# Optimization experiments

Measured on AMD Instinct MI355X. Metric: run time of the kernel, lower is better.

## Reference

```python
import jax, jax.numpy as jnp
import numpy as np

B, L, V, D, C, R = 8, 2048, 32000, 512, 64, 64
NBLK = 2           # n_layers - 1
H = 2 * D          # stem hidden dim
STD = 0.02


def _ln(x, w, b):
    m = x.mean(-1, keepdims=True)
    v = ((x - m) ** 2).mean(-1, keepdims=True)
    return (x - m) / jnp.sqrt(v + 1e-5) * w + b


def setup_inputs() -> dict:
    key = jax.random.key(0)
    ks = jax.random.split(key, 16)
    n = lambda k, shp: jax.random.normal(k, shp, dtype=jnp.float32) * STD
    return {
        "token_ids": jax.random.randint(ks[0], (B, L), 0, V),
        "tok_emb": n(ks[1], (V, D)),
        "pos_emb": n(ks[2], (L, D)),
        "stem_ln_w": jnp.ones((NBLK, D), jnp.float32),
        "stem_ln_b": jnp.zeros((NBLK, D), jnp.float32),
        "stem_w1": n(ks[3], (NBLK, D, H)),
        "stem_b1": jnp.zeros((NBLK, H), jnp.float32),
        "stem_w2": n(ks[4], (NBLK, H, D)),
        "stem_b2": jnp.zeros((NBLK, D), jnp.float32),
        "role_ln_w": jnp.ones((D,), jnp.float32),
        "role_ln_b": jnp.zeros((D,), jnp.float32),
        "Wa": n(ks[5], (D, R)),
        "Wb": n(ks[6], (D, R)),
        "Wc": n(ks[7], (D, R)),
        "class_a": n(ks[8], (C, R)),
        "class_b": n(ks[9], (C, R)),
        "class_c": n(ks[10], (C, R)),
        "query_ln_w": jnp.ones((D,), jnp.float32),
        "query_ln_b": jnp.zeros((D,), jnp.float32),
        "Wq": n(ks[11], (D, C)),
        "bq": jnp.zeros((C,), jnp.float32),
    }


def reference(token_ids, tok_emb, pos_emb, stem_ln_w, stem_ln_b, stem_w1,
              stem_b1, stem_w2, stem_b2, role_ln_w, role_ln_b, Wa, Wb, Wc,
              class_a, class_b, class_c, query_ln_w, query_ln_b, Wq, bq):
    seq_len = token_ids.shape[1]
    x = tok_emb[token_ids] + pos_emb[:seq_len][None, :, :]  # [B,L,D]
    for i in range(NBLK):
        h = _ln(x, stem_ln_w[i], stem_ln_b[i])
        h = jax.nn.gelu(h @ stem_w1[i] + stem_b1[i], approximate=False)
        x = x + h @ stem_w2[i] + stem_b2[i]
    prefix = _ln(x[:, :-1], role_ln_w, role_ln_b)  # [B,L-1,D]
    a = jnp.tanh(prefix @ Wa)
    b = jnp.tanh(prefix @ Wb)
    c = jnp.tanh(prefix @ Wc)
    ua = jnp.einsum('blr,cr->blc', a, class_a)  # [B,L-1,C]
    ub = jnp.einsum('blr,cr->blc', b, class_b)
    uc = jnp.einsum('blr,cr->blc', c, class_c)
    # exact ordered-triplet sum  sum_{i<j<k} ua_i * ub_j * uc_k  via exclusive cumsums
    prefA = jnp.cumsum(ua, axis=1) - ua            # sum_{i<j} ua_i
    t = ub * prefA
    prefT = jnp.cumsum(t, axis=1) - t              # sum_{j<k} ub_j * prefA_j
    s = (uc * prefT).sum(axis=1)                   # [B,C]
    Lp = max(seq_len - 1, 1)
    denom = max(Lp * (Lp - 1) * (Lp - 2) / 6.0, 1.0)
    q = _ln(x[:, -1], query_ln_w, query_ln_b)
    return s / denom + q @ Wq + bq
```

## Files before the change

### kernel.cpp

```cpp
#include <hip/hip_runtime.h>

#define NROWS 16384
#define LSEQ  2048
#define NB    8

typedef short v8s __attribute__((ext_vector_type(8)));
typedef float v4f __attribute__((ext_vector_type(4)));

__device__ __forceinline__ unsigned short f2bf(float f) {
    unsigned int u = __float_as_uint(f);
    return (unsigned short)((u + 0x7fffu + ((u >> 16) & 1u)) >> 16);
}
__device__ __forceinline__ float bf2f(unsigned short u) {
    return __uint_as_float(((unsigned int)u) << 16);
}

__device__ __forceinline__ float fast_gelu(float v) {
    float z = fabsf(v) * 0.70710678118654752f;
    float t = __builtin_amdgcn_rcpf(1.0f + 0.3275911f * z);
    float poly = t * (0.254829592f + t * (-0.284496736f + t * (1.421413741f +
                 t * (-1.453152027f + t * 1.061405429f))));
    float erfz = 1.0f - poly * __expf(-z * z);
    float er = copysignf(erfz, v);
    return 0.5f * v * (1.0f + er);
}
__device__ __forceinline__ float fast_tanh(float y) {
    float e = __expf(2.0f * y);
    return (e - 1.0f) * __builtin_amdgcn_rcpf(e + 1.0f);
}

__global__ __launch_bounds__(256) void setup_kernel(
        const int* __restrict__ ids,
        const float* __restrict__ tok, const float* __restrict__ pos,
        const float* __restrict__ g0, const float* __restrict__ b0,
        unsigned short* __restrict__ x, unsigned short* __restrict__ hl,
        const float* __restrict__ w1, const float* __restrict__ w2,
        const float* __restrict__ wa, const float* __restrict__ wb, const float* __restrict__ wc,
        const float* __restrict__ ca, const float* __restrict__ cb, const float* __restrict__ cc,
        unsigned short* __restrict__ w1T, unsigned short* __restrict__ w2T,
        unsigned short* __restrict__ wabcT, unsigned short* __restrict__ clsb) {
    int blk = blockIdx.x;
    int t = threadIdx.x;
    if (blk < 4096) {
        int wave = t >> 6, lane = t & 63;
        long row = (long)blk * 4 + wave;
        int l = (int)(row & (LSEQ - 1));
        int id = ids[row];
        int d = lane * 8;
        float4 t0 = *(const float4*)(tok + (size_t)id * 512 + d);
        float4 t1 = *(const float4*)(tok + (size_t)id * 512 + d + 4);
        float4 p0 = *(const float4*)(pos + (size_t)l * 512 + d);
        float4 p1 = *(const float4*)(pos + (size_t)l * 512 + d + 4);
        float a[8] = {t0.x + p0.x, t0.y + p0.y, t0.z + p0.z, t0.w + p0.w,
                      t1.x + p1.x, t1.y + p1.y, t1.z + p1.z, t1.w + p1.w};
        unsigned int xp[4];
        #pragma unroll
        for (int i = 0; i < 4; ++i)
            xp[i] = (unsigned int)f2bf(a[2 * i]) | ((unsigned int)f2bf(a[2 * i + 1]) << 16);
        *(uint4*)(x + row * 512 + d) = *(uint4*)xp;
        float s = 0.f, s2 = 0.f;
        #pragma unroll
        for (int i = 0; i < 8; ++i) { s += a[i]; s2 += a[i] * a[i]; }
        #pragma unroll
        for (int o = 32; o > 0; o >>= 1) { s += __shfl_down(s, o); s2 += __shfl_down(s2, o); }
        s = __shfl(s, 0); s2 = __shfl(s2, 0);
        float m = s * (1.0f / 512.0f);
        float rinv = 1.0f / sqrtf(s2 * (1.0f / 512.0f) - m * m + 1e-5f);
        float4 ga = *(const float4*)(g0 + d), gb = *(const float4*)(g0 + d + 4);
        float4 ba = *(const float4*)(b0 + d), bb2 = *(const float4*)(b0 + d + 4);
        float gg[8] = {ga.x, ga.y, ga.z, ga.w, gb.x, gb.y, gb.z, gb.w};
        float bb[8] = {ba.x, ba.y, ba.z, ba.w, bb2.x, bb2.y, bb2.z, bb2.w};
        unsigned int hp[4];
        #pragma unroll
        for (int i = 0; i < 4; ++i) {
            unsigned short lo = f2bf((a[2 * i]     - m) * rinv * gg[2 * i]     + bb[2 * i]);
            unsigned short hi = f2bf((a[2 * i + 1] - m) * rinv * gg[2 * i + 1] + bb[2 * i + 1]);
            hp[i] = (unsigned int)lo | ((unsigned int)hi << 16);
        }
        *(uint4*)(hl + row * 512 + d) = *(uint4*)hp;
    } else if (blk < 6240) {
        int id = blk - 4096;
        int tx = t & 31, ty = t >> 5;
        const float* in; unsigned short* out; int R, C, bx, by, ldo;
        if (id < 1024) {
            int l = id >> 9, r = id & 511;
            in = w1 + l * 524288; out = w1T + l * 524288;
            R = 512; C = 1024; bx = r & 31; by = r >> 5; ldo = 512;
        } else if (id < 2048) {
            int l = (id - 1024) >> 9, r = (id - 1024) & 511;
            in = w2 + l * 524288; out = w2T + l * 524288;
            R = 1024; C = 512; bx = r & 15; by = r >> 4; ldo = 1024;
        } else {
            int g = (id - 2048) >> 5, r = (id - 2048) & 31;
            in = (g == 0) ? wa : (g == 1) ? wb : wc;
            out = wabcT + g * 32768;
            R = 512; C = 64; bx = r & 1; by = r >> 1; ldo = 512;
        }
        __shared__ unsigned short tile[32][33];
        int c0 = bx * 32, r0 = by * 32;
        for (int i = ty; i < 32; i += 8) {
            int r = r0 + i, c = c0 + tx;
            tile[i][tx] = (r < R && c < C) ? f2bf(in[(size_t)r * C + c]) : (unsigned short)0;
        }
        __syncthreads();
        for (int i = ty; i < 32; i += 8) {
            int c = c0 + i, r = r0 + tx;
            if (r < R && c < C) out[(size_t)c * ldo + r] = tile[tx][i];
        }
    } else {
        int g = blk - 6240;
        const float* src = (g == 0) ? ca : (g == 1) ? cb : cc;
        unsigned short* dst = clsb + g * 4096;
        for (int i = t; i < 4096; i += 256) dst[i] = f2bf(src[i]);
    }
}

__global__ __launch_bounds__(256) void ln_kernel(const unsigned short* __restrict__ x,
        const float* __restrict__ g, const float* __restrict__ b,
        unsigned short* __restrict__ out) {
    int wave = threadIdx.x >> 6, lane = threadIdx.x & 63;
    long row = (long)blockIdx.x * 4 + wave;
    int d = lane * 8;
    uint4 xp = *(const uint4*)(x + row * 512 + d);
    const unsigned int* xw = (const unsigned int*)&xp;
    float a[8];
    #pragma unroll
    for (int i = 0; i < 4; ++i) {
        a[2 * i]     = bf2f((unsigned short)(xw[i] & 0xffff));
        a[2 * i + 1] = bf2f((unsigned short)(xw[i] >> 16));
    }
    float s = 0.f, s2 = 0.f;
    #pragma unroll
    for (int i = 0; i < 8; ++i) { s += a[i]; s2 += a[i] * a[i]; }
    #pragma unroll
    for (int o = 32; o > 0; o >>= 1) { s += __shfl_down(s, o); s2 += __shfl_down(s2, o); }
    s = __shfl(s, 0); s2 = __shfl(s2, 0);
    float m = s * (1.0f / 512.0f);
    float rinv = 1.0f / sqrtf(s2 * (1.0f / 512.0f) - m * m + 1e-5f);
    float4 g0 = *(const float4*)(g + d), g1 = *(const float4*)(g + d + 4);
    float4 b0 = *(const float4*)(b + d), b1 = *(const float4*)(b + d + 4);
    float gg[8] = {g0.x, g0.y, g0.z, g0.w, g1.x, g1.y, g1.z, g1.w};
    float bb[8] = {b0.x, b0.y, b0.z, b0.w, b1.x, b1.y, b1.z, b1.w};
    unsigned int hp[4];
    #pragma unroll
    for (int i = 0; i < 4; ++i) {
        unsigned short lo = f2bf((a[2 * i]     - m) * rinv * gg[2 * i]     + bb[2 * i]);
        unsigned short hi = f2bf((a[2 * i + 1] - m) * rinv * gg[2 * i + 1] + bb[2 * i + 1]);
        hp[i] = (unsigned int)lo | ((unsigned int)hi << 16);
    }
    *(uint4*)(out + row * 512 + d) = *(uint4*)hp;
}

#define EPI_GELU_BF16  0
#define EPI_RES_BF16   1

template <int EPI, int TN>
__global__ __launch_bounds__(256) void gemm_r2(
        const unsigned short* __restrict__ A, int lda,
        const unsigned short* __restrict__ BT, int ldb,
        const float* __restrict__ bias,
        const unsigned short* __restrict__ xres,
        unsigned short* __restrict__ Cout, int ldc, int K) {
    constexpr int NJ = TN / 32;
    __shared__ unsigned short As[128][40] __attribute__((aligned(16)));
    __shared__ unsigned short Bs[TN][40] __attribute__((aligned(16)));
    const int t = threadIdx.x;
    const int lane = t & 63, wave = t >> 6;
    const int quad = lane >> 4, l16 = lane & 15;
    const int wm = (wave >> 1) * 64, wn = (wave & 1) * (TN / 2);
    const long tileM = (long)blockIdx.x * 128, tileN = (long)blockIdx.y * TN;
    const int arow = t >> 2, acol = (t & 3) * 8;

    const unsigned short* gA0 = A + (tileM + arow) * lda + acol;
    const unsigned short* gA1 = gA0 + 64 * (long)lda;
    const unsigned short* gB0 = BT + (tileN + arow) * ldb + acol;
    const unsigned short* gB1 = gB0 + 64 * (long)ldb;

    v4f acc[4][NJ] = {};
    uint4 a0, a1, b0, b1;

    a0 = *(const uint4*)gA0; a1 = *(const uint4*)gA1; gA0 += 32; gA1 += 32;
    b0 = *(const uint4*)gB0; gB0 += 32;
    if (TN == 128) { b1 = *(const uint4*)gB1; gB1 += 32; }
    *(uint4*)&As[arow][acol] = a0;
    *(uint4*)&As[arow + 64][acol] = a1;
    *(uint4*)&Bs[arow][acol] = b0;
    if (TN == 128) *(uint4*)&Bs[arow + 64][acol] = b1;

    const int nk = K >> 5;
    for (int kk = 0; kk < nk; ++kk) {
        __syncthreads();
        const bool more = kk + 1 < nk;
        if (more) {
            a0 = *(const uint4*)gA0; a1 = *(const uint4*)gA1; gA0 += 32; gA1 += 32;
            b0 = *(const uint4*)gB0; gB0 += 32;
            if (TN == 128) { b1 = *(const uint4*)gB1; gB1 += 32; }
        }
        v8s af[4], bfr[NJ];
        #pragma unroll
        for (int i = 0; i < 4; ++i) af[i] = *(const v8s*)&As[wm + i * 16 + l16][quad * 8];
        #pragma unroll
        for (int j = 0; j < NJ; ++j) bfr[j] = *(const v8s*)&Bs[wn + j * 16 + l16][quad * 8];
        #pragma unroll
        for (int i = 0; i < 4; ++i)
            #pragma unroll
            for (int j = 0; j < NJ; ++j)
                acc[i][j] = __builtin_amdgcn_mfma_f32_16x16x32_bf16(bfr[j], af[i], acc[i][j], 0, 0, 0);
        __syncthreads();
        if (more) {
            *(uint4*)&As[arow][acol] = a0;
            *(uint4*)&As[arow + 64][acol] = a1;
            *(uint4*)&Bs[arow][acol] = b0;
            if (TN == 128) *(uint4*)&Bs[arow + 64][acol] = b1;
        }
    }

    #pragma unroll
    for (int i = 0; i < 4; ++i) {
        long m = tileM + wm + i * 16 + l16;
        #pragma unroll
        for (int j = 0; j < NJ; ++j) {
            long n0 = tileN + wn + j * 16 + quad * 4;
            float4 bi = *(const float4*)&bias[n0];
            const float* bip = (const float*)&bi;
            unsigned short pk[4];
            if (EPI == EPI_GELU_BF16) {
                #pragma unroll
                for (int r = 0; r < 4; ++r)
                    pk[r] = f2bf(fast_gelu(acc[i][j][r] + bip[r]));
            } else {
                ushort4 xr4 = *(const ushort4*)&xres[m * ldc + n0];
                const unsigned short* xp = (const unsigned short*)&xr4;
                #pragma unroll
                for (int r = 0; r < 4; ++r)
                    pk[r] = f2bf(acc[i][j][r] + bip[r] + bf2f(xp[r]));
            }
            *(ushort4*)&Cout[m * ldc + n0] = *(ushort4*)pk;
        }
    }
}

__global__ __launch_bounds__(256) void tanh_class_kernel(
        const unsigned short* __restrict__ A,
        const unsigned short* __restrict__ WT,
        const unsigned short* __restrict__ cls,
        unsigned short* __restrict__ uu) {
    __shared__ unsigned short As[128][40] __attribute__((aligned(16)));
    __shared__ unsigned short Bs[64][40] __attribute__((aligned(16)));
    __shared__ unsigned short P[128 * 72] __attribute__((aligned(16)));
    const int t = threadIdx.x;
    const int lane = t & 63, wave = t >> 6;
    const int quad = lane >> 4, l16 = lane & 15;
    const int wm = (wave >> 1) * 64, wn = (wave & 1) * 32;
    const long tileM = (long)blockIdx.x * 128;
    const int g = blockIdx.y;
    const int arow = t >> 2, acol = (t & 3) * 8;

    const unsigned short* BT = WT + g * 32768;
    v8s cf[2][2];
    #pragma unroll
    for (int ks = 0; ks < 2; ++ks)
        #pragma unroll
        for (int j = 0; j < 2; ++j)
            cf[ks][j] = *(const v8s*)&cls[g * 4096 + (wn + j * 16 + l16) * 64 + ks * 32 + quad * 8];

    const unsigned short* gA0 = A + (tileM + arow) * 512 + acol;
    const unsigned short* gA1 = gA0 + 64 * 512;
    const unsigned short* gB0 = BT + arow * 512 + acol;

    v4f acc[4][2] = {};
    uint4 a0, a1, b0;
    a0 = *(const uint4*)gA0; a1 = *(const uint4*)gA1; gA0 += 32; gA1 += 32;
    b0 = *(const uint4*)gB0; gB0 += 32;
    *(uint4*)&As[arow][acol] = a0;
    *(uint4*)&As[arow + 64][acol] = a1;
    *(uint4*)&Bs[arow][acol] = b0;

    for (int kk = 0; kk < 16; ++kk) {
        __syncthreads();
        const bool more = kk < 15;
        if (more) {
            a0 = *(const uint4*)gA0; a1 = *(const uint4*)gA1; gA0 += 32; gA1 += 32;
            b0 = *(const uint4*)gB0; gB0 += 32;
        }
        v8s af[4], bfr[2];
        #pragma unroll
        for (int i = 0; i < 4; ++i) af[i] = *(const v8s*)&As[wm + i * 16 + l16][quad * 8];
        #pragma unroll
        for (int j = 0; j < 2; ++j) bfr[j] = *(const v8s*)&Bs[wn + j * 16 + l16][quad * 8];
        #pragma unroll
        for (int i = 0; i < 4; ++i)
            #pragma unroll
            for (int j = 0; j < 2; ++j)
                acc[i][j] = __builtin_amdgcn_mfma_f32_16x16x32_bf16(bfr[j], af[i], acc[i][j], 0, 0, 0);
        __syncthreads();
        if (more) {
            *(uint4*)&As[arow][acol] = a0;
            *(uint4*)&As[arow + 64][acol] = a1;
            *(uint4*)&Bs[arow][acol] = b0;
        }
    }

    #pragma unroll
    for (int i = 0; i < 4; ++i) {
        int m = wm + i * 16 + l16;
        #pragma unroll
        for (int j = 0; j < 2; ++j) {
            int n0 = wn + j * 16 + quad * 4;
            unsigned short pk[4];
            #pragma unroll
            for (int r = 0; r < 4; ++r) pk[r] = f2bf(fast_tanh(acc[i][j][r]));
            *(ushort4*)&P[m * 72 + n0] = *(ushort4*)pk;
        }
    }
    __syncthreads();

    v4f acc2[4][2] = {};
    #pragma unroll
    for (int ks = 0; ks < 2; ++ks) {
        v8s paf[4];
        #pragma unroll
        for (int i = 0; i < 4; ++i)
            paf[i] = *(const v8s*)&P[(wm + i * 16 + l16) * 72 + ks * 32 + quad * 8];
        #pragma unroll
        for (int i = 0; i < 4; ++i)
            #pragma unroll
            for (int j = 0; j < 2; ++j)
                acc2[i][j] = __builtin_amdgcn_mfma_f32_16x16x32_bf16(cf[ks][j], paf[i], acc2[i][j], 0, 0, 0);
    }

    #pragma unroll
    for (int i = 0; i < 4; ++i) {
        long m = tileM + wm + i * 16 + l16;
        #pragma unroll
        for (int j = 0; j < 2; ++j) {
            int c0 = wn + j * 16 + quad * 4;
            unsigned short pk[4];
            #pragma unroll
            for (int r = 0; r < 4; ++r) pk[r] = f2bf(acc2[i][j][r]);
            *(ushort4*)&uu[m * 192 + g * 64 + c0] = *(ushort4*)pk;
        }
    }
}

__global__ __launch_bounds__(64) void scan_part_kernel(const unsigned short* __restrict__ u,
                                                       float* __restrict__ part) {
    int b = blockIdx.x, seg = blockIdx.y;
    int c = threadIdx.x;
    int l0 = seg * 32;
    int l1 = l0 + 32; if (l1 > 2047) l1 = 2047;
    float sA = 0.f, sB = 0.f, sC = 0.f, T = 0.f, M = 0.f, U = 0.f;
    const unsigned short* base = u + ((size_t)b * LSEQ + l0) * 192 + c;
    for (int l = l0; l < l1; ++l) {
        float ua = bf2f(base[0]), ub = bf2f(base[64]), uc = bf2f(base[128]);
        base += 192;
        U += uc * T;
        M += uc * sB;
        T += ub * sA;
        sA += ua; sB += ub; sC += uc;
    }
    float* p = part + ((size_t)(b * 64 + seg)) * 384 + c;
    p[0] = sA; p[64] = sB; p[128] = sC; p[192] = T; p[256] = M; p[320] = U;
}

__global__ __launch_bounds__(64) void combine_final_kernel(const float* __restrict__ part,
        const unsigned short* __restrict__ x,
        const float* __restrict__ qw, const float* __restrict__ qb,
        const float* __restrict__ Wq, const float* __restrict__ bq,
        float* __restrict__ out, float inv_denom) {
    int b = blockIdx.x;
    int c = threadIdx.x;
    const float* p = part + (size_t)b * 64 * 384 + c;
    float A = p[0], B = p[64], Tt = p[192], Mt = p[256], Ut = p[320];
    for (int seg = 1; seg < 64; ++seg) {
        const float* q2 = p + seg * 384;
        float a2 = q2[0], b2 = q2[64], c2 = q2[128], t2 = q2[192], m2 = q2[256], u2 = q2[320];
        float Un = Ut + u2 + c2 * Tt + A * m2;
        float Tn = Tt + t2 + A * b2;
        float Mn = Mt + m2 + B * c2;
        A += a2; B += b2;
        Ut = Un; Tt = Tn; Mt = Mn;
    }
    __shared__ float q[512];
    __shared__ float mv[2];
    const unsigned short* xr = x + ((size_t)b * LSEQ + (LSEQ - 1)) * 512;
    float s1 = 0.f, s2 = 0.f;
    for (int i = c; i < 512; i += 64) { float v = bf2f(xr[i]); q[i] = v; s1 += v; s2 += v * v; }
    #pragma unroll
    for (int o = 32; o > 0; o >>= 1) { s1 += __shfl_down(s1, o); s2 += __shfl_down(s2, o); }
    if (c == 0) {
        float m = s1 * (1.0f / 512.0f);
        float var = s2 * (1.0f / 512.0f) - m * m;
        mv[0] = m; mv[1] = 1.0f / sqrtf(var + 1e-5f);
    }
    __syncthreads();
    float m = mv[0], r = mv[1];
    for (int i = c; i < 512; i += 64) q[i] = (q[i] - m) * r * qw[i] + qb[i];
    __syncthreads();
    float acc = 0.f;
    for (int d = 0; d < 512; ++d) acc += q[d] * Wq[d * 64 + c];
    out[b * 64 + c] = Ut * inv_denom + acc + bq[c];
}

extern "C" void kernel_launch(void* const* d_in, const int* in_sizes, int n_in,
                              void* d_out, int out_size, void* d_ws, size_t ws_size,
                              hipStream_t stream) {
    const int*   token_ids   = (const int*)d_in[0];
    const float* tok_emb     = (const float*)d_in[1];
    const float* pos_emb     = (const float*)d_in[2];
    const float* stem_ln_w   = (const float*)d_in[3];
    const float* stem_ln_b   = (const float*)d_in[4];
    const float* stem_w1     = (const float*)d_in[5];
    const float* stem_b1     = (const float*)d_in[6];
    const float* stem_w2     = (const float*)d_in[7];
    const float* stem_b2     = (const float*)d_in[8];
    const float* role_ln_w   = (const float*)d_in[9];
    const float* role_ln_b   = (const float*)d_in[10];
    const float* Wa          = (const float*)d_in[11];
    const float* Wb          = (const float*)d_in[12];
    const float* Wc          = (const float*)d_in[13];
    const float* class_a     = (const float*)d_in[14];
    const float* class_b     = (const float*)d_in[15];
    const float* class_c     = (const float*)d_in[16];
    const float* query_ln_w  = (const float*)d_in[17];
    const float* query_ln_b  = (const float*)d_in[18];
    const float* Wq          = (const float*)d_in[19];
    const float* bq          = (const float*)d_in[20];
    float* out = (float*)d_out;

    char* wsb = (char*)d_ws;
    unsigned short* x    = (unsigned short*)(wsb);
    unsigned short* hl   = (unsigned short*)(wsb + 16777216);
    unsigned short* Hb   = (unsigned short*)(wsb + 33554432);
    unsigned short* uu   = (unsigned short*)(wsb + 67108864);
    float* part          = (float*)(wsb + 73400320);
    unsigned short* w1T  = (unsigned short*)(wsb + 74188800);
    unsigned short* w2T  = (unsigned short*)(wsb + 76285952);
    unsigned short* wabcT= (unsigned short*)(wsb + 78383104);
    unsigned short* clsb = (unsigned short*)(wsb + 78579712);

    setup_kernel<<<6243, 256, 0, stream>>>(token_ids, tok_emb, pos_emb,
        stem_ln_w, stem_ln_b, x, hl,
        stem_w1, stem_w2, Wa, Wb, Wc, class_a, class_b, class_c,
        w1T, w2T, wabcT, clsb);

    for (int i = 0; i < 2; ++i) {
        if (i > 0)
            ln_kernel<<<NROWS / 4, 256, 0, stream>>>(x, stem_ln_w + 512, stem_ln_b + 512, hl);
        gemm_r2<EPI_GELU_BF16, 128><<<dim3(128, 8), 256, 0, stream>>>(
            hl, 512, w1T + i * 524288, 512, stem_b1 + i * 1024, nullptr, Hb, 1024, 512);
        gemm_r2<EPI_RES_BF16, 64><<<dim3(128, 8), 256, 0, stream>>>(
            Hb, 1024, w2T + i * 524288, 1024, stem_b2 + i * 512, x, x, 512, 1024);
    }

    ln_kernel<<<NROWS / 4, 256, 0, stream>>>(x, role_ln_w, role_ln_b, hl);

    tanh_class_kernel<<<dim3(128, 3), 256, 0, stream>>>(hl, wabcT, clsb, uu);

    scan_part_kernel<<<dim3(NB, 64), 64, 0, stream>>>(uu, part);

    float inv_denom = (float)(6.0 / (2047.0 * 2046.0 * 2045.0));
    combine_final_kernel<<<NB, 64, 0, stream>>>(part, x, query_ln_w, query_ln_b,
                                                Wq, bq, out, inv_denom);
}
```

Before: 343.4 us.

## Fuse LayerNorm into GEMM prologues by folding gamma/beta into weights

Removes the standalone LayerNorm kernels and the hl intermediate buffer. LayerNorm gamma is folded into the transposed weights and beta is precomputed into the biases during setup, so the GEMMs only need the per-row mean and rstd. Each GEMM block computes these statistics from x in a prologue and normalizes A tiles as it loads them. The cost is that every N-tile block recomputes the row statistics (8x redundant reads of x for W1, 3x for the tanh/class kernel), and the bias precompute loops run serially in setup.

```diff
diff --git a/kernel.cpp b/kernel.cpp
--- a/kernel.cpp
+++ b/kernel.cpp
@@ -29,16 +29,31 @@
     return (e - 1.0f) * __builtin_amdgcn_rcpf(e + 1.0f);
 }
 
+__device__ __forceinline__ uint4 ln8(uint4 v, float m, float r) {
+    const unsigned int* vw = (const unsigned int*)&v;
+    unsigned int o[4];
+    #pragma unroll
+    for (int k = 0; k < 4; ++k) {
+        float f0 = (bf2f((unsigned short)(vw[k] & 0xffff)) - m) * r;
+        float f1 = (bf2f((unsigned short)(vw[k] >> 16)) - m) * r;
+        o[k] = (unsigned int)f2bf(f0) | ((unsigned int)f2bf(f1) << 16);
+    }
+    return *(uint4*)o;
+}
+
 __global__ __launch_bounds__(256) void setup_kernel(
         const int* __restrict__ ids,
         const float* __restrict__ tok, const float* __restrict__ pos,
-        const float* __restrict__ g0, const float* __restrict__ b0,
-        unsigned short* __restrict__ x, unsigned short* __restrict__ hl,
+        unsigned short* __restrict__ x,
         const float* __restrict__ w1, const float* __restrict__ w2,
         const float* __restrict__ wa, const float* __restrict__ wb, const float* __restrict__ wc,
         const float* __restrict__ ca, const float* __restrict__ cb, const float* __restrict__ cc,
+        const float* __restrict__ lnw, const float* __restrict__ lnb,
+        const float* __restrict__ sb1,
+        const float* __restrict__ rlw, const float* __restrict__ rlb,
         unsigned short* __restrict__ w1T, unsigned short* __restrict__ w2T,
-        unsigned short* __restrict__ wabcT, unsigned short* __restrict__ clsb) {
+        unsigned short* __restrict__ wabcT, unsigned short* __restrict__ clsb,
+        float* __restrict__ b1p, float* __restrict__ babc) {
     int blk = blockIdx.x;
     int t = threadIdx.x;
     if (blk < 4096) {
@@ -58,33 +73,14 @@
         for (int i = 0; i < 4; ++i)
             xp[i] = (unsigned int)f2bf(a[2 * i]) | ((unsigned int)f2bf(a[2 * i + 1]) << 16);
         *(uint4*)(x + row * 512 + d) = *(uint4*)xp;
-        float s = 0.f, s2 = 0.f;
-        #pragma unroll
-        for (int i = 0; i < 8; ++i) { s += a[i]; s2 += a[i] * a[i]; }
-        #pragma unroll
-        for (int o = 32; o > 0; o >>= 1) { s += __shfl_down(s, o); s2 += __shfl_down(s2, o); }
-        s = __shfl(s, 0); s2 = __shfl(s2, 0);
-        float m = s * (1.0f / 512.0f);
-        float rinv = 1.0f / sqrtf(s2 * (1.0f / 512.0f) - m * m + 1e-5f);
-        float4 ga = *(const float4*)(g0 + d), gb = *(const float4*)(g0 + d + 4);
-        float4 ba = *(const float4*)(b0 + d), bb2 = *(const float4*)(b0 + d + 4);
-        float gg[8] = {ga.x, ga.y, ga.z, ga.w, gb.x, gb.y, gb.z, gb.w};
-        float bb[8] = {ba.x, ba.y, ba.z, ba.w, bb2.x, bb2.y, bb2.z, bb2.w};
-        unsigned int hp[4];
-        #pragma unroll
-        for (int i = 0; i < 4; ++i) {
-            unsigned short lo = f2bf((a[2 * i]     - m) * rinv * gg[2 * i]     + bb[2 * i]);
-            unsigned short hi = f2bf((a[2 * i + 1] - m) * rinv * gg[2 * i + 1] + bb[2 * i + 1]);
-            hp[i] = (unsigned int)lo | ((unsigned int)hi << 16);
-        }
-        *(uint4*)(hl + row * 512 + d) = *(uint4*)hp;
     } else if (blk < 6240) {
         int id = blk - 4096;
         int tx = t & 31, ty = t >> 5;
         const float* in; unsigned short* out; int R, C, bx, by, ldo;
+        const float* sc = nullptr;
         if (id < 1024) {
             int l = id >> 9, r = id & 511;
-            in = w1 + l * 524288; out = w1T + l * 524288;
+            in = w1 + l * 524288; out = w1T + l * 524288; sc = lnw + l * 512;
             R = 512; C = 1024; bx = r & 31; by = r >> 5; ldo = 512;
         } else if (id < 2048) {
             int l = (id - 1024) >> 9, r = (id - 1024) & 511;
@@ -93,125 +89,127 @@
         } else {
             int g = (id - 2048) >> 5, r = (id - 2048) & 31;
             in = (g == 0) ? wa : (g == 1) ? wb : wc;
-            out = wabcT + g * 32768;
+            out = wabcT + g * 32768; sc = rlw;
             R = 512; C = 64; bx = r & 1; by = r >> 1; ldo = 512;
         }
         __shared__ unsigned short tile[32][33];
         int c0 = bx * 32, r0 = by * 32;
         for (int i = ty; i < 32; i += 8) {
             int r = r0 + i, c = c0 + tx;
-            tile[i][tx] = (r < R && c < C) ? f2bf(in[(size_t)r * C + c]) : (unsigned short)0;
+            if (r < R && c < C) {
+                float f = in[(size_t)r * C + c];
+                if (sc) f *= sc[r];
+                tile[i][tx] = f2bf(f);
+            } else tile[i][tx] = 0;
         }
         __syncthreads();
         for (int i = ty; i < 32; i += 8) {
             int c = c0 + i, r = r0 + tx;
             if (r < R && c < C) out[(size_t)c * ldo + r] = tile[tx][i];
         }
-    } else {
+    } else if (blk < 6243) {
         int g = blk - 6240;
         const float* src = (g == 0) ? ca : (g == 1) ? cb : cc;
         unsigned short* dst = clsb + g * 4096;
         for (int i = t; i < 4096; i += 256) dst[i] = f2bf(src[i]);
-    }
-}
-
-__global__ __launch_bounds__(256) void ln_kernel(const unsigned short* __restrict__ x,
-        const float* __restrict__ g, const float* __restrict__ b,
-        unsigned short* __restrict__ out) {
-    int wave = threadIdx.x >> 6, lane = threadIdx.x & 63;
-    long row = (long)blockIdx.x * 4 + wave;
-    int d = lane * 8;
-    uint4 xp = *(const uint4*)(x + row * 512 + d);
-    const unsigned int* xw = (const unsigned int*)&xp;
-    float a[8];
-    #pragma unroll
-    for (int i = 0; i < 4; ++i) {
-        a[2 * i]     = bf2f((unsigned short)(xw[i] & 0xffff));
-        a[2 * i + 1] = bf2f((unsigned short)(xw[i] >> 16));
-    }
-    float s = 0.f, s2 = 0.f;
-    #pragma unroll
-    for (int i = 0; i < 8; ++i) { s += a[i]; s2 += a[i] * a[i]; }
-    #pragma unroll
-    for (int o = 32; o > 0; o >>= 1) { s += __shfl_down(s, o); s2 += __shfl_down(s2, o); }
-    s = __shfl(s, 0); s2 = __shfl(s2, 0);
-    float m = s * (1.0f / 512.0f);
-    float rinv = 1.0f / sqrtf(s2 * (1.0f / 512.0f) - m * m + 1e-5f);
-    float4 g0 = *(const float4*)(g + d), g1 = *(const float4*)(g + d + 4);
-    float4 b0 = *(const float4*)(b + d), b1 = *(const float4*)(b + d + 4);
-    float gg[8] = {g0.x, g0.y, g0.z, g0.w, g1.x, g1.y, g1.z, g1.w};
-    float bb[8] = {b0.x, b0.y, b0.z, b0.w, b1.x, b1.y, b1.z, b1.w};
-    unsigned int hp[4];
-    #pragma unroll
-    for (int i = 0; i < 4; ++i) {
-        unsigned short lo = f2bf((a[2 * i]     - m) * rinv * gg[2 * i]     + bb[2 * i]);
-        unsigned short hi = f2bf((a[2 * i + 1] - m) * rinv * gg[2 * i + 1] + bb[2 * i + 1]);
-        hp[i] = (unsigned int)lo | ((unsigned int)hi << 16);
-    }
-    *(uint4*)(out + row * 512 + d) = *(uint4*)hp;
-}
-
-#define EPI_GELU_BF16  0
-#define EPI_RES_BF16   1
-
-template <int EPI, int TN>
-__global__ __launch_bounds__(256) void gemm_r2(
-        const unsigned short* __restrict__ A, int lda,
-        const unsigned short* __restrict__ BT, int ldb,
+    } else if (blk < 6251) {
+        int gidx = (blk - 6243) * 256 + t;
+        int i = gidx >> 10, n = gidx & 1023;
+        float sum = sb1[i * 1024 + n];
+        const float* lb = lnb + i * 512;
+        const float* wp = w1 + i * 524288 + n;
+        for (int c = 0; c < 512; ++c) sum += lb[c] * wp[(size_t)c * 1024];
+        b1p[gidx] = sum;
+    } else {
+        if (t < 192) {
+            int g = t >> 6, r = t & 63;
+            const float* wp = ((g == 0) ? wa : (g == 1) ? wb : wc) + r;
+            float sum = 0.f;
+            for (int c = 0; c < 512; ++c) sum += rlb[c] * wp[(size_t)c * 64];
+            babc[t] = sum;
+        }
+    }
+}
+
+__global__ __launch_bounds__(256) void gemm_w1ln(
+        const unsigned short* __restrict__ X,
+        const unsigned short* __restrict__ BT,
         const float* __restrict__ bias,
-        const unsigned short* __restrict__ xres,
-        unsigned short* __restrict__ Cout, int ldc, int K) {
-    constexpr int NJ = TN / 32;
+        unsigned short* __restrict__ Cout) {
     __shared__ unsigned short As[128][40] __attribute__((aligned(16)));
-    __shared__ unsigned short Bs[TN][40] __attribute__((aligned(16)));
+    __shared__ unsigned short Bs[128][40] __attribute__((aligned(16)));
+    __shared__ float mS[128], rSS[128];
     const int t = threadIdx.x;
     const int lane = t & 63, wave = t >> 6;
     const int quad = lane >> 4, l16 = lane & 15;
-    const int wm = (wave >> 1) * 64, wn = (wave & 1) * (TN / 2);
-    const long tileM = (long)blockIdx.x * 128, tileN = (long)blockIdx.y * TN;
+    const int wm = (wave >> 1) * 64, wn = (wave & 1) * 64;
+    const long tileM = (long)blockIdx.x * 128, tileN = (long)blockIdx.y * 128;
     const int arow = t >> 2, acol = (t & 3) * 8;
 
-    const unsigned short* gA0 = A + (tileM + arow) * lda + acol;
-    const unsigned short* gA1 = gA0 + 64 * (long)lda;
-    const unsigned short* gB0 = BT + (tileN + arow) * ldb + acol;
-    const unsigned short* gB1 = gB0 + 64 * (long)ldb;
-
-    v4f acc[4][NJ] = {};
+    {
+        int sr = t >> 1, sh = t & 1;
+        const unsigned short* xr = X + (tileM + sr) * 512 + sh * 256;
+        float s = 0.f, s2 = 0.f;
+        #pragma unroll 8
+        for (int q = 0; q < 32; ++q) {
+            uint4 v = *(const uint4*)(xr + q * 8);
+            const unsigned int* vw = (const unsigned int*)&v;
+            #pragma unroll
+            for (int k = 0; k < 4; ++k) {
+                float f0 = bf2f((unsigned short)(vw[k] & 0xffff));
+                float f1 = bf2f((unsigned short)(vw[k] >> 16));
+                s += f0 + f1; s2 += f0 * f0 + f1 * f1;
+            }
+        }
+        s += __shfl_xor(s, 1); s2 += __shfl_xor(s2, 1);
+        if (sh == 0) {
+            float m = s * (1.0f / 512.0f);
+            mS[sr] = m;
+            rSS[sr] = 1.0f / sqrtf(s2 * (1.0f / 512.0f) - m * m + 1e-5f);
+        }
+    }
+    __syncthreads();
+    const float m0 = mS[arow],      r0 = rSS[arow];
+    const float m1 = mS[arow + 64], r1 = rSS[arow + 64];
+
+    const unsigned short* gA0 = X + (tileM + arow) * 512 + acol;
+    const unsigned short* gA1 = gA0 + 64 * 512;
+    const unsigned short* gB0 = BT + (tileN + arow) * 512 + acol;
+    const unsigned short* gB1 = gB0 + 64 * 512;
+
+    v4f acc[4][4] = {};
     uint4 a0, a1, b0, b1;
 
     a0 = *(const uint4*)gA0; a1 = *(const uint4*)gA1; gA0 += 32; gA1 += 32;
-    b0 = *(const uint4*)gB0; gB0 += 32;
-    if (TN == 128) { b1 = *(const uint4*)gB1; gB1 += 32; }
-    *(uint4*)&As[arow][acol] = a0;
-    *(uint4*)&As[arow + 64][acol] = a1;
-    *(uint4*)&Bs[arow][acol] = b0;
-    if (TN == 128) *(uint4*)&Bs[arow + 64][acol] = b1;
-
-    const int nk = K >> 5;
-    for (int kk = 0; kk < nk; ++kk) {
-        __syncthreads();
-        const bool more = kk + 1 < nk;
+    b0 = *(const uint4*)gB0; b1 = *(const uint4*)gB1; gB0 += 32; gB1 += 32;
+    *(uint4*)&As[arow][acol]      = ln8(a0, m0, r0);
+    *(uint4*)&As[arow + 64][acol] = ln8(a1, m1, r1);
+    *(uint4*)&Bs[arow][acol]      = b0;
+    *(uint4*)&Bs[arow + 64][acol] = b1;
+
+    for (int kk = 0; kk < 16; ++kk) {
+        __syncthreads();
+        const bool more = kk < 15;
         if (more) {
             a0 = *(const uint4*)gA0; a1 = *(const uint4*)gA1; gA0 += 32; gA1 += 32;
-            b0 = *(const uint4*)gB0; gB0 += 32;
-            if (TN == 128) { b1 = *(const uint4*)gB1; gB1 += 32; }
-        }
-        v8s af[4], bfr[NJ];
+            b0 = *(const uint4*)gB0; b1 = *(const uint4*)gB1; gB0 += 32; gB1 += 32;
+        }
+        v8s af[4], bfr[4];
         #pragma unroll
         for (int i = 0; i < 4; ++i) af[i] = *(const v8s*)&As[wm + i * 16 + l16][quad * 8];
         #pragma unroll
-        for (int j = 0; j < NJ; ++j) bfr[j] = *(const v8s*)&Bs[wn + j * 16 + l16][quad * 8];
+        for (int j = 0; j < 4; ++j) bfr[j] = *(const v8s*)&Bs[wn + j * 16 + l16][quad * 8];
         #pragma unroll
         for (int i = 0; i < 4; ++i)
             #pragma unroll
-            for (int j = 0; j < NJ; ++j)
+            for (int j = 0; j < 4; ++j)
                 acc[i][j] = __builtin_amdgcn_mfma_f32_16x16x32_bf16(bfr[j], af[i], acc[i][j], 0, 0, 0);
         __syncthreads();
         if (more) {
-            *(uint4*)&As[arow][acol] = a0;
-            *(uint4*)&As[arow + 64][acol] = a1;
-            *(uint4*)&Bs[arow][acol] = b0;
-            if (TN == 128) *(uint4*)&Bs[arow + 64][acol] = b1;
+            *(uint4*)&As[arow][acol]      = ln8(a0, m0, r0);
+            *(uint4*)&As[arow + 64][acol] = ln8(a1, m1, r1);
+            *(uint4*)&Bs[arow][acol]      = b0;
+            *(uint4*)&Bs[arow + 64][acol] = b1;
         }
     }
 
@@ -219,35 +217,99 @@
     for (int i = 0; i < 4; ++i) {
         long m = tileM + wm + i * 16 + l16;
         #pragma unroll
-        for (int j = 0; j < NJ; ++j) {
+        for (int j = 0; j < 4; ++j) {
             long n0 = tileN + wn + j * 16 + quad * 4;
             float4 bi = *(const float4*)&bias[n0];
             const float* bip = (const float*)&bi;
             unsigned short pk[4];
-            if (EPI == EPI_GELU_BF16) {
-                #pragma unroll
-                for (int r = 0; r < 4; ++r)
-                    pk[r] = f2bf(fast_gelu(acc[i][j][r] + bip[r]));
-            } else {
-                ushort4 xr4 = *(const ushort4*)&xres[m * ldc + n0];
-                const unsigned short* xp = (const unsigned short*)&xr4;
-                #pragma unroll
-                for (int r = 0; r < 4; ++r)
-                    pk[r] = f2bf(acc[i][j][r] + bip[r] + bf2f(xp[r]));
-            }
-            *(ushort4*)&Cout[m * ldc + n0] = *(ushort4*)pk;
+            #pragma unroll
+            for (int r = 0; r < 4; ++r)
+                pk[r] = f2bf(fast_gelu(acc[i][j][r] + bip[r]));
+            *(ushort4*)&Cout[m * 1024 + n0] = *(ushort4*)pk;
+        }
+    }
+}
+
+__global__ __launch_bounds__(256) void gemm_w2(
+        const unsigned short* __restrict__ A,
+        const unsigned short* __restrict__ BT,
+        const float* __restrict__ bias,
+        unsigned short* __restrict__ Xio) {
+    __shared__ unsigned short As[128][40] __attribute__((aligned(16)));
+    __shared__ unsigned short Bs[64][40] __attribute__((aligned(16)));
+    const int t = threadIdx.x;
+    const int lane = t & 63, wave = t >> 6;
+    const int quad = lane >> 4, l16 = lane & 15;
+    const int wm = (wave >> 1) * 64, wn = (wave & 1) * 32;
+    const long tileM = (long)blockIdx.x * 128, tileN = (long)blockIdx.y * 64;
+    const int arow = t >> 2, acol = (t & 3) * 8;
+
+    const unsigned short* gA0 = A + (tileM + arow) * 1024 + acol;
+    const unsigned short* gA1 = gA0 + 64 * 1024;
+    const unsigned short* gB0 = BT + (tileN + arow) * 1024 + acol;
+    v4f acc[4][2] = {};
+    uint4 a0, a1, b0;
+
+    a0 = *(const uint4*)gA0; a1 = *(const uint4*)gA1; gA0 += 32; gA1 += 32;
+    b0 = *(const uint4*)gB0; gB0 += 32;
+    *(uint4*)&As[arow][acol] = a0;
+    *(uint4*)&As[arow + 64][acol] = a1;
+    if (arow < 64) *(uint4*)&Bs[arow][acol] = b0;
+
+    for (int kk = 0; kk < 32; ++kk) {
+        __syncthreads();
+        const bool more = kk < 31;
+        if (more) {
+            a0 = *(const uint4*)gA0; a1 = *(const uint4*)gA1; gA0 += 32; gA1 += 32;
+            b0 = *(const uint4*)gB0; gB0 += 32;
+        }
+        v8s af[4], bfr[2];
+        #pragma unroll
+        for (int i = 0; i < 4; ++i) af[i] = *(const v8s*)&As[wm + i * 16 + l16][quad * 8];
+        #pragma unroll
+        for (int j = 0; j < 2; ++j) bfr[j] = *(const v8s*)&Bs[wn + j * 16 + l16][quad * 8];
+        #pragma unroll
+        for (int i = 0; i < 4; ++i)
+            #pragma unroll
+            for (int j = 0; j < 2; ++j)
+                acc[i][j] = __builtin_amdgcn_mfma_f32_16x16x32_bf16(bfr[j], af[i], acc[i][j], 0, 0, 0);
+        __syncthreads();
+        if (more) {
+            *(uint4*)&As[arow][acol] = a0;
+            *(uint4*)&As[arow + 64][acol] = a1;
+            if (arow < 64) *(uint4*)&Bs[arow][acol] = b0;
+        }
+    }
+
+    #pragma unroll
+    for (int i = 0; i < 4; ++i) {
+        long m = tileM + wm + i * 16 + l16;
+        #pragma unroll
+        for (int j = 0; j < 2; ++j) {
+            long n0 = tileN + wn + j * 16 + quad * 4;
+            float4 bi = *(const float4*)&bias[n0];
+            const float* bip = (const float*)&bi;
+            ushort4 xr4 = *(const ushort4*)&Xio[m * 512 + n0];
+            const unsigned short* xp = (const unsigned short*)&xr4;
+            unsigned short pk[4];
+            #pragma unroll
+            for (int r = 0; r < 4; ++r)
+                pk[r] = f2bf(acc[i][j][r] + bip[r] + bf2f(xp[r]));
+            *(ushort4*)&Xio[m * 512 + n0] = *(ushort4*)pk;
         }
     }
 }
 
 __global__ __launch_bounds__(256) void tanh_class_kernel(
-        const unsigned short* __restrict__ A,
+        const unsigned short* __restrict__ X,
         const unsigned short* __restrict__ WT,
         const unsigned short* __restrict__ cls,
+        const float* __restrict__ babc,
         unsigned short* __restrict__ uu) {
     __shared__ unsigned short As[128][40] __attribute__((aligned(16)));
     __shared__ unsigned short Bs[64][40] __attribute__((aligned(16)));
     __shared__ unsigned short P[128 * 72] __attribute__((aligned(16)));
+    __shared__ float mS[128], rSS[128];
     const int t = threadIdx.x;
     const int lane = t & 63, wave = t >> 6;
     const int quad = lane >> 4, l16 = lane & 15;
@@ -256,6 +318,32 @@
     const int g = blockIdx.y;
     const int arow = t >> 2, acol = (t & 3) * 8;
 
+    {
+        int sr = t >> 1, sh = t & 1;
+        const unsigned short* xr = X + (tileM + sr) * 512 + sh * 256;
+        float s = 0.f, s2 = 0.f;
+        #pragma unroll 8
+        for (int q = 0; q < 32; ++q) {
+            uint4 v = *(const uint4*)(xr + q * 8);
+            const unsigned int* vw = (const unsigned int*)&v;
+            #pragma unroll
+            for (int k = 0; k < 4; ++k) {
+                float f0 = bf2f((unsigned short)(vw[k] & 0xffff));
+                float f1 = bf2f((unsigned short)(vw[k] >> 16));
+                s += f0 + f1; s2 += f0 * f0 + f1 * f1;
+            }
+        }
+        s += __shfl_xor(s, 1); s2 += __shfl_xor(s2, 1);
+        if (sh == 0) {
+            float m = s * (1.0f / 512.0f);
+            mS[sr] = m;
+            rSS[sr] = 1.0f / sqrtf(s2 * (1.0f / 512.0f) - m * m + 1e-5f);
+        }
+    }
+    __syncthreads();
+    const float m0 = mS[arow],      r0 = rSS[arow];
+    const float m1 = mS[arow + 64], r1 = rSS[arow + 64];
+
     const unsigned short* BT = WT + g * 32768;
     v8s cf[2][2];
     #pragma unroll
@@ -264,7 +352,7 @@
         for (int j = 0; j < 2; ++j)
             cf[ks][j] = *(const v8s*)&cls[g * 4096 + (wn + j * 16 + l16) * 64 + ks * 32 + quad * 8];
 
-    const unsigned short* gA0 = A + (tileM + arow) * 512 + acol;
+    const unsigned short* gA0 = X + (tileM + arow) * 512 + acol;
     const unsigned short* gA1 = gA0 + 64 * 512;
     const unsigned short* gB0 = BT + arow * 512 + acol;
 
@@ -272,9 +360,9 @@
     uint4 a0, a1, b0;
     a0 = *(const uint4*)gA0; a1 = *(const uint4*)gA1; gA0 += 32; gA1 += 32;
     b0 = *(const uint4*)gB0; gB0 += 32;
-    *(uint4*)&As[arow][acol] = a0;
-    *(uint4*)&As[arow + 64][acol] = a1;
-    *(uint4*)&Bs[arow][acol] = b0;
+    *(uint4*)&As[arow][acol] = ln8(a0, m0, r0);
+    *(uint4*)&As[arow + 64][acol] = ln8(a1, m1, r1);
+    if (arow < 64) *(uint4*)&Bs[arow][acol] = b0;
 
     for (int kk = 0; kk < 16; ++kk) {
         __syncthreads();
@@ -295,9 +383,9 @@
                 acc[i][j] = __builtin_amdgcn_mfma_f32_16x16x32_bf16(bfr[j], af[i], acc[i][j], 0, 0, 0);
         __syncthreads();
         if (more) {
-            *(uint4*)&As[arow][acol] = a0;
-            *(uint4*)&As[arow + 64][acol] = a1;
-            *(uint4*)&Bs[arow][acol] = b0;
+            *(uint4*)&As[arow][acol] = ln8(a0, m0, r0);
+            *(uint4*)&As[arow + 64][acol] = ln8(a1, m1, r1);
+            if (arow < 64) *(uint4*)&Bs[arow][acol] = b0;
         }
     }
 
@@ -307,9 +395,11 @@
         #pragma unroll
         for (int j = 0; j < 2; ++j) {
             int n0 = wn + j * 16 + quad * 4;
+            float4 bi = *(const float4*)&babc[g * 64 + n0];
+            const float* bip = (const float*)&bi;
             unsigned short pk[4];
             #pragma unroll
-            for (int r = 0; r < 4; ++r) pk[r] = f2bf(fast_tanh(acc[i][j][r]));
+            for (int r = 0; r < 4; ++r) pk[r] = f2bf(fast_tanh(acc[i][j][r] + bip[r]));
             *(ushort4*)&P[m * 72 + n0] = *(ushort4*)pk;
         }
     }
@@ -430,32 +520,29 @@
 
     char* wsb = (char*)d_ws;
     unsigned short* x    = (unsigned short*)(wsb);
-    unsigned short* hl   = (unsigned short*)(wsb + 16777216);
-    unsigned short* Hb   = (unsigned short*)(wsb + 33554432);
-    unsigned short* uu   = (unsigned short*)(wsb + 67108864);
-    float* part          = (float*)(wsb + 73400320);
-    unsigned short* w1T  = (unsigned short*)(wsb + 74188800);
-    unsigned short* w2T  = (unsigned short*)(wsb + 76285952);
-    unsigned short* wabcT= (unsigned short*)(wsb + 78383104);
-    unsigned short* clsb = (unsigned short*)(wsb + 78579712);
-
-    setup_kernel<<<6243, 256, 0, stream>>>(token_ids, tok_emb, pos_emb,
-        stem_ln_w, stem_ln_b, x, hl,
+    unsigned short* Hb   = (unsigned short*)(wsb + 16777216);
+    unsigned short* uu   = (unsigned short*)(wsb + 50331648);
+    float* part          = (float*)(wsb + 56623104);
+    unsigned short* w1T  = (unsigned short*)(wsb + 57409536);
+    unsigned short* w2T  = (unsigned short*)(wsb + 59506688);
+    unsigned short* wabcT= (unsigned short*)(wsb + 61603840);
+    unsigned short* clsb = (unsigned short*)(wsb + 61800448);
+    float* b1p           = (float*)(wsb + 61825024);
+    float* babc          = (float*)(wsb + 61833216);
+
+    setup_kernel<<<6252, 256, 0, stream>>>(token_ids, tok_emb, pos_emb, x,
         stem_w1, stem_w2, Wa, Wb, Wc, class_a, class_b, class_c,
-        w1T, w2T, wabcT, clsb);
+        stem_ln_w, stem_ln_b, stem_b1, role_ln_w, role_ln_b,
+        w1T, w2T, wabcT, clsb, b1p, babc);
 
     for (int i = 0; i < 2; ++i) {
-        if (i > 0)
-            ln_kernel<<<NROWS / 4, 256, 0, stream>>>(x, stem_ln_w + 512, stem_ln_b + 512, hl);
-        gemm_r2<EPI_GELU_BF16, 128><<<dim3(128, 8), 256, 0, stream>>>(
-            hl, 512, w1T + i * 524288, 512, stem_b1 + i * 1024, nullptr, Hb, 1024, 512);
-        gemm_r2<EPI_RES_BF16, 64><<<dim3(128, 8), 256, 0, stream>>>(
-            Hb, 1024, w2T + i * 524288, 1024, stem_b2 + i * 512, x, x, 512, 1024);
-    }
-
-    ln_kernel<<<NROWS / 4, 256, 0, stream>>>(x, role_ln_w, role_ln_b, hl);
-
-    tanh_class_kernel<<<dim3(128, 3), 256, 0, stream>>>(hl, wabcT, clsb, uu);
+        gemm_w1ln<<<dim3(128, 8), 256, 0, stream>>>(
+            x, w1T + i * 524288, b1p + i * 1024, Hb);
+        gemm_w2<<<dim3(128, 8), 256, 0, stream>>>(
+            Hb, w2T + i * 524288, stem_b2 + i * 512, x);
+    }
+
+    tanh_class_kernel<<<dim3(128, 3), 256, 0, stream>>>(x, wabcT, clsb, babc, uu);
 
     scan_part_kernel<<<dim3(NB, 64), 64, 0, stream>>>(uu, part);
 
```

After: 394.9 us. 1.15x slower.
